# Kernel optimization log

Measured on AMD Instinct MI355X. Metric: run time of the kernel, lower is better.

The kernel has to match this reference:

```python
import jax, jax.numpy as jnp
import numpy as np
from jax import lax


def _conv(x, w, b, stride, pad):
    y = lax.conv_general_dilated(
        x, w, window_strides=(stride, stride),
        padding=[(pad, pad), (pad, pad)],
        dimension_numbers=('NCHW', 'OIHW', 'NCHW'))
    return y + b[None, :, None, None]


def _maxpool3s2(x):
    return lax.reduce_window(x, -jnp.inf, lax.max,
                             (1, 1, 3, 3), (1, 1, 2, 2), 'VALID')


def setup_inputs() -> dict:
    key = jax.random.key(0)
    ks = jax.random.split(key, 16)
    s = 0.05  # weight scale for numerical sanity
    inp = {
        'x': jax.random.normal(ks[0], (128, 3, 224, 224), jnp.float32),
        'w1': jax.random.normal(ks[1], (64, 3, 3, 3), jnp.float32) * s,
        'b1': jnp.zeros((64,), jnp.float32),
        'w2': jax.random.normal(ks[2], (192, 64, 5, 5), jnp.float32) * s,
        'b2': jnp.zeros((192,), jnp.float32),
        'w3': jax.random.normal(ks[3], (384, 192, 3, 3), jnp.float32) * s,
        'b3': jnp.zeros((384,), jnp.float32),
        'w4': jax.random.normal(ks[4], (256, 384, 3, 3), jnp.float32) * s,
        'b4': jnp.zeros((256,), jnp.float32),
        'w5': jax.random.normal(ks[5], (256, 256, 3, 3), jnp.float32) * s,
        'b5': jnp.zeros((256,), jnp.float32),
        'fc1_w': jax.random.normal(ks[6], (4096, 9216), jnp.float32) * 0.01,
        'fc1_b': jnp.zeros((4096,), jnp.float32),
        'fc2_w': jax.random.normal(ks[7], (4096, 4096), jnp.float32) * 0.01,
        'fc2_b': jnp.zeros((4096,), jnp.float32),
        'fc3_w': jax.random.normal(ks[8], (10, 4096), jnp.float32) * 0.01,
        'fc3_b': jnp.zeros((10,), jnp.float32),
        # uniform(0.1, 0.3) per element, matching random.uniform(0.1, 0.3)
        'unif': jax.random.uniform(ks[9], (128, 10), jnp.float32, 0.1, 0.3),
        # np.random.normal(0, 1) noise
        'noise': jax.random.normal(ks[10], (128, 10), jnp.float32),
    }
    return inp


def _forward(x, w1, b1, w2, b2, w3, b3, w4, b4, w5, b5,
             fc1_w, fc1_b, fc2_w, fc2_b, fc3_w, fc3_b, unif, noise):
    # features
    h = jax.nn.relu(_conv(x, w1, b1, stride=4, pad=2))   # [B,64,57,57]
    h = _maxpool3s2(h)                                   # [B,64,28,28]
    h = jax.nn.relu(_conv(h, w2, b2, stride=1, pad=2))   # [B,192,28,28]
    h = _maxpool3s2(h)                                   # [B,192,13,13]
    h = jax.nn.relu(_conv(h, w3, b3, stride=1, pad=1))   # [B,384,13,13]
    h = jax.nn.relu(_conv(h, w4, b4, stride=1, pad=1))   # [B,256,13,13]
    h = jax.nn.relu(_conv(h, w5, b5, stride=1, pad=1))   # [B,256,13,13]
    h = _maxpool3s2(h)                                   # [B,256,6,6]
    # adaptive avgpool to (6,6) is identity at this spatial size
    h = h.reshape(h.shape[0], 256 * 6 * 6)               # [B,9216]
    # classifier (Dropout = identity in eval mode)
    h = jax.nn.relu(h @ fc1_w.T + fc1_b)                 # [B,4096]
    h = jax.nn.relu(h @ fc2_w.T + fc2_b)                 # [B,4096]
    logits = h @ fc3_w.T + fc3_b                         # [B,10]
    # post: keep argmax entry, replace others with unif*max (detached),
    # add Gaussian noise, softmax
    m = jnp.max(logits, axis=-1, keepdims=True)          # [B,1]
    idx = jnp.argmax(logits, axis=-1, keepdims=True)     # first max, like torch
    onehot = jnp.arange(logits.shape[-1])[None, :] == idx
    filled = jnp.where(onehot, logits, unif * lax.stop_gradient(m))
    return jax.nn.softmax(filled + noise, axis=-1)


def reference(x, w1, b1, w2, b2, w3, b3, w4, b4, w5, b5,
              fc1_w, fc1_b, fc2_w, fc2_b, fc3_w, fc3_b, unif, noise):
    return _forward(x, w1, b1, w2, b2, w3, b3, w4, b4, w5, b5,
                    fc1_w, fc1_b, fc2_w, fc2_b, fc3_w, fc3_b, unif, noise)
```

## Files before the change

kernel.cpp:

```cpp
#include <hip/hip_runtime.h>
#include <math.h>


typedef __attribute__((ext_vector_type(4))) float  f32x4;
typedef __attribute__((ext_vector_type(8))) short  bf16x8;

#define OFF_C1O      25690112ull
#define OFF_X2H      0ull
#define OFF_X2L      12845056ull
#define OFF_WT2H     25690112ull
#define OFF_WT2L     26304512ull
#define OFF_WT3H     26918912ull
#define OFF_WT3L     28246016ull
#define OFF_WT4H     29573120ull
#define OFF_WT4L     31342592ull
#define OFF_WT5H     33112064ull
#define OFF_WT5L     34291712ull
#define OFF_Y2H      36000000ull
#define OFF_Y2L      74535168ull
#define OFF_X3H      113100000ull
#define OFF_X3L      121406688ull
#define OFF_Y3H      36000000ull
#define OFF_Y3L      52613376ull
#define OFF_Y4H      70000000ull
#define OFF_Y4L      81075584ull
#define OFF_Y5H      93000000ull
#define OFF_Y5L      104075584ull
#define OFF_P3       0ull
#define OFF_FC1      5000000ull
#define OFF_FC2      8000000ull
#define OFF_LOG      11000000ull
#define OFF_PART     40000000ull

__device__ inline void bf16split(float v, unsigned short& h, unsigned short& l) {
  unsigned u = __builtin_bit_cast(unsigned, v);
  unsigned hb = (u + 0x7fffu + ((u >> 16) & 1u)) >> 16;
  h = (unsigned short)hb;
  float hf = __builtin_bit_cast(float, hb << 16);
  float r = v - hf;
  unsigned u2 = __builtin_bit_cast(unsigned, r);
  l = (unsigned short)((u2 + 0x7fffu + ((u2 >> 16) & 1u)) >> 16);
}
__device__ inline void bf16split_fast(float v, unsigned short& h, unsigned short& l) {
  unsigned u = __builtin_bit_cast(unsigned, v);
  h = (unsigned short)(u >> 16);
  float r = v - __builtin_bit_cast(float, u & 0xFFFF0000u);
  unsigned u2 = __builtin_bit_cast(unsigned, r);
  l = (unsigned short)((u2 + 0x7fffu + ((u2 >> 16) & 1u)) >> 16);
}
__device__ inline float bf2f(unsigned short h) {
  return __builtin_bit_cast(float, ((unsigned)h) << 16);
}

__global__ __launch_bounds__(256) void conv1_kernel(
    const float* __restrict__ x, const float* __restrict__ w,
    const float* __restrict__ bias, float* __restrict__ out) {
  const int b = blockIdx.y;
  const int s = blockIdx.x * 256 + threadIdx.x;
  if (s >= 57 * 57) return;
  const int oh = s / 57, ow = s % 57;
  float iv[27];
#pragma unroll
  for (int ci = 0; ci < 3; ++ci)
#pragma unroll
    for (int kh = 0; kh < 3; ++kh)
#pragma unroll
      for (int kw = 0; kw < 3; ++kw) {
        const int ih = oh * 4 - 2 + kh;
        const int iw = ow * 4 - 2 + kw;
        float v = 0.f;
        if (ih >= 0 && ih < 224 && iw >= 0 && iw < 224)
          v = x[(((size_t)b * 3 + ci) * 224 + ih) * 224 + iw];
        iv[ci * 9 + kh * 3 + kw] = v;
      }
  for (int co = 0; co < 64; ++co) {
    float a = bias[co];
#pragma unroll
    for (int p = 0; p < 27; ++p) a = fmaf(w[co * 27 + p], iv[p], a);
    out[((size_t)b * 64 + co) * 3249 + s] = fmaxf(a, 0.f);
  }
}

__global__ __launch_bounds__(256) void pool1cvt_kernel(
    const float* __restrict__ in, unsigned short* __restrict__ xh,
    unsigned short* __restrict__ xl) {
  const int tid = blockIdx.x * 256 + threadIdx.x;
  if (tid >= 128 * 784) return;
  const int b = tid / 784, s = tid % 784;
  const int oh = s / 28, ow = s % 28;
  const float* base = in + (size_t)b * 64 * 3249 + (size_t)(oh * 2) * 57 + ow * 2;
  for (int cg = 0; cg < 16; ++cg) {
    unsigned short h[4], l[4];
#pragma unroll
    for (int j = 0; j < 4; ++j) {
      const float* p = base + (size_t)(cg * 4 + j) * 3249;
      float m = -INFINITY;
#pragma unroll
      for (int kh = 0; kh < 3; ++kh)
#pragma unroll
        for (int kw = 0; kw < 3; ++kw) m = fmaxf(m, p[kh * 57 + kw]);
      bf16split(m, h[j], l[j]);
    }
    const size_t g = ((size_t)b * 784 + s) * 64 + cg * 4;
    *reinterpret_cast<uint2*>(xh + g) =
        make_uint2((unsigned)h[0] | ((unsigned)h[1] << 16),
                   (unsigned)h[2] | ((unsigned)h[3] << 16));
    *reinterpret_cast<uint2*>(xl + g) =
        make_uint2((unsigned)l[0] | ((unsigned)l[1] << 16),
                   (unsigned)l[2] | ((unsigned)l[3] << 16));
  }
}

__global__ void wtrans_hl_kernel(const float* __restrict__ w,
                                 unsigned short* __restrict__ wh,
                                 unsigned short* __restrict__ wl,
                                 int C_in, int P, int C_out) {
  const int ncc = C_in >> 5;
  const int total = C_out * P * C_in;
  for (int e = blockIdx.x * blockDim.x + threadIdx.x; e < total;
       e += gridDim.x * blockDim.x) {
    const int ci_in = e & 31;
    int t1 = e >> 5;
    const int fr = t1 & 15;
    int t2 = t1 >> 4;
    const int cc = t2 % ncc;
    int t3 = t2 / ncc;
    const int p = t3 % P;
    const int ct = t3 / P;
    const int co = ct * 16 + fr;
    const int ci = cc * 32 + ci_in;
    const float v = w[((size_t)co * C_in + ci) * P + p];
    unsigned short h, l;
    bf16split(v, h, l);
    wh[e] = h; wl[e] = l;
  }
}

__global__ __launch_bounds__(256, 2) void conv2_mfma_kernel(
    const unsigned short* __restrict__ xh, const unsigned short* __restrict__ xl,
    const unsigned short* __restrict__ wh, const unsigned short* __restrict__ wl,
    const float* __restrict__ bias,
    unsigned short* __restrict__ yh, unsigned short* __restrict__ yl) {
  __shared__ unsigned short xt_h[352 * 40];
  __shared__ unsigned short xt_l[352 * 40];
  const int t = threadIdx.x;
  const int lane = t & 63, wv = t >> 6;
  const int b = blockIdx.x;
  const int rg = blockIdx.y;
  const int cg = blockIdx.z;
  const int fr = lane & 15, fq = lane >> 4;
  const int k0 = fq * 8;
  const int frag = fr * 32 + k0;

  int bofs[4];
  bool act[4];
#pragma unroll
  for (int ti = 0; ti < 4; ++ti) {
    const int tile = ti * 4 + wv;
    act[ti] = (tile <= 12);
    int n = tile * 16 + fr;
    if (tile > 12 || n > 195) n = 195;
    const int r = n / 28, c = n % 28;
    bofs[ti] = (r * 32 + c) * 40 + k0;
  }

  f32x4 acc[4][4];
#pragma unroll
  for (int i = 0; i < 4; ++i)
#pragma unroll
    for (int j = 0; j < 4; ++j) acc[i][j] = (f32x4){0.f, 0.f, 0.f, 0.f};

  for (int cc = 0; cc < 2; ++cc) {
    __syncthreads();
    for (int e = t; e < 1408; e += 256) {
      const int sp = e >> 2, kg = e & 3;
      const int hr = sp >> 5, hc = sp & 31;
      const int ih = rg * 7 + hr - 2, ic = hc - 2;
      uint4 vh = make_uint4(0, 0, 0, 0), vl = make_uint4(0, 0, 0, 0);
      if (ih >= 0 && ih < 28 && ic >= 0 && ic < 28) {
        const size_t g = ((size_t)b * 784 + ih * 28 + ic) * 64 + cc * 32 + kg * 8;
        vh = *reinterpret_cast<const uint4*>(xh + g);
        vl = *reinterpret_cast<const uint4*>(xl + g);
      }
      *reinterpret_cast<uint4*>(xt_h + sp * 40 + kg * 8) = vh;
      *reinterpret_cast<uint4*>(xt_l + sp * 40 + kg * 8) = vl;
    }
    __syncthreads();
#pragma unroll 5
    for (int p = 0; p < 25; ++p) {
      bf16x8 a_h[4], a_l[4];
#pragma unroll
      for (int cot = 0; cot < 4; ++cot) {
        const size_t wg = ((((size_t)(cg * 4 + cot) * 25 + p) * 2 + cc) << 9) + frag;
        a_h[cot] = __builtin_bit_cast(bf16x8, *reinterpret_cast<const uint4*>(wh + wg));
        a_l[cot] = __builtin_bit_cast(bf16x8, *reinterpret_cast<const uint4*>(wl + wg));
      }
      const int kh = p / 5, kw = p % 5;
      const int poff = (kh * 32 + kw) * 40;
      bf16x8 bh[4], bl[4];
#pragma unroll
      for (int ti = 0; ti < 4; ++ti) {
        if (act[ti]) {
          bh[ti] = __builtin_bit_cast(bf16x8,
              *reinterpret_cast<const uint4*>(xt_h + bofs[ti] + poff));
          bl[ti] = __builtin_bit_cast(bf16x8,
              *reinterpret_cast<const uint4*>(xt_l + bofs[ti] + poff));
        }
      }
#pragma unroll
      for (int ti = 0; ti < 4; ++ti) if (act[ti])
#pragma unroll
        for (int cot = 0; cot < 4; ++cot)
          acc[ti][cot] = __builtin_amdgcn_mfma_f32_16x16x32_bf16(a_h[cot], bh[ti], acc[ti][cot], 0, 0, 0);
#pragma unroll
      for (int ti = 0; ti < 4; ++ti) if (act[ti])
#pragma unroll
        for (int cot = 0; cot < 4; ++cot)
          acc[ti][cot] = __builtin_amdgcn_mfma_f32_16x16x32_bf16(a_h[cot], bl[ti], acc[ti][cot], 0, 0, 0);
#pragma unroll
      for (int ti = 0; ti < 4; ++ti) if (act[ti])
#pragma unroll
        for (int cot = 0; cot < 4; ++cot)
          acc[ti][cot] = __builtin_amdgcn_mfma_f32_16x16x32_bf16(a_l[cot], bh[ti], acc[ti][cot], 0, 0, 0);
    }
  }
#pragma unroll
  for (int cot = 0; cot < 4; ++cot) {
    const int co = cg * 64 + cot * 16 + fq * 4;
    const float4 bi = *reinterpret_cast<const float4*>(bias + co);
    const float bia[4] = {bi.x, bi.y, bi.z, bi.w};
#pragma unroll
    for (int ti = 0; ti < 4; ++ti) {
      const int tile = ti * 4 + wv;
      if (tile > 12) continue;
      const int n = tile * 16 + fr;
      if (n > 195) continue;
      const int oh = rg * 7 + n / 28, ow = n % 28;
      unsigned short h[4], l[4];
#pragma unroll
      for (int r = 0; r < 4; ++r) {
        const float v = fmaxf(acc[ti][cot][r] + bia[r], 0.f);
        bf16split(v, h[r], l[r]);
      }
      const size_t g = ((size_t)b * 784 + oh * 28 + ow) * 192 + co;
      *reinterpret_cast<uint2*>(yh + g) =
          make_uint2((unsigned)h[0] | ((unsigned)h[1] << 16),
                     (unsigned)h[2] | ((unsigned)h[3] << 16));
      *reinterpret_cast<uint2*>(yl + g) =
          make_uint2((unsigned)l[0] | ((unsigned)l[1] << 16),
                     (unsigned)l[2] | ((unsigned)l[3] << 16));
    }
  }
}

__global__ __launch_bounds__(256) void pool2_hl_kernel(
    const unsigned short* __restrict__ yh, const unsigned short* __restrict__ yl,
    unsigned short* __restrict__ xh, unsigned short* __restrict__ xl) {
  const int tid = blockIdx.x * 256 + threadIdx.x;
  if (tid >= 128 * 169 * 48) return;
  const int c4 = tid % 48;
  const int r = tid / 48;
  const int s = r % 169;
  const int b = r / 169;
  const int oh = s / 13, ow = s % 13;
  float m[4] = {-INFINITY, -INFINITY, -INFINITY, -INFINITY};
#pragma unroll
  for (int kh = 0; kh < 3; ++kh) {
#pragma unroll
    for (int kw = 0; kw < 3; ++kw) {
      const int si = (oh * 2 + kh) * 28 + (ow * 2 + kw);
      const size_t g = ((size_t)b * 784 + si) * 192 + c4 * 4;
      const uint2 vh = *reinterpret_cast<const uint2*>(yh + g);
      const uint2 vl = *reinterpret_cast<const uint2*>(yl + g);
      const unsigned hw[2] = {vh.x, vh.y}, lw[2] = {vl.x, vl.y};
#pragma unroll
      for (int j = 0; j < 4; ++j) {
        const float v = bf2f((unsigned short)(hw[j >> 1] >> ((j & 1) * 16))) +
                        bf2f((unsigned short)(lw[j >> 1] >> ((j & 1) * 16)));
        m[j] = fmaxf(m[j], v);
      }
    }
  }
  unsigned short h[4], l[4];
#pragma unroll
  for (int j = 0; j < 4; ++j) bf16split(m[j], h[j], l[j]);
  const size_t gd = ((size_t)b * 169 + s) * 192 + c4 * 4;
  *reinterpret_cast<uint2*>(xh + gd) =
      make_uint2((unsigned)h[0] | ((unsigned)h[1] << 16),
                 (unsigned)h[2] | ((unsigned)h[3] << 16));
  *reinterpret_cast<uint2*>(xl + gd) =
      make_uint2((unsigned)l[0] | ((unsigned)l[1] << 16),
                 (unsigned)l[2] | ((unsigned)l[3] << 16));
}

__global__ __launch_bounds__(256, 4) void conv13_mfma_kernel(
    const unsigned short* __restrict__ xh, const unsigned short* __restrict__ xl,
    const unsigned short* __restrict__ wh, const unsigned short* __restrict__ wl,
    const float* __restrict__ bias,
    unsigned short* __restrict__ yh, unsigned short* __restrict__ yl,
    int C_in, int C_out) {
  __shared__ unsigned short xt_h[225 * 40];
  __shared__ unsigned short xt_l[225 * 40];
  const int t = threadIdx.x;
  const int lane = t & 63;
  const int wv = t >> 6;
  const int b = blockIdx.x;
  const int co0 = blockIdx.y * 64 + wv * 16;
  const int ctile = blockIdx.y * 4 + wv;
  const int fr = lane & 15;
  const int fq = lane >> 4;
  const int k0 = fq * 8;
  const int frag = fr * 32 + k0;

  int bofs[11];
#pragma unroll
  for (int nt = 0; nt < 11; ++nt) {
    int n = nt * 16 + fr;
    if (n > 168) n = 168;
    const int oh = n / 13, ow = n % 13;
    bofs[nt] = (oh * 15 + ow) * 40 + k0;
  }

  f32x4 acc[11];
#pragma unroll
  for (int nt = 0; nt < 11; ++nt) acc[nt] = (f32x4){0.f, 0.f, 0.f, 0.f};

  const int ncc = C_in >> 5;
  for (int cc = 0; cc < ncc; ++cc) {
    __syncthreads();
    for (int e = t; e < 900; e += 256) {
      const int sp = e >> 2, kg = e & 3;
      const int r = sp / 15, c = sp % 15;
      const int ir = r - 1, ic = c - 1;
      uint4 vh = make_uint4(0, 0, 0, 0), vl = make_uint4(0, 0, 0, 0);
      if (ir >= 0 && ir < 13 && ic >= 0 && ic < 13) {
        const size_t g = ((size_t)b * 169 + ir * 13 + ic) * C_in + cc * 32 + kg * 8;
        vh = *reinterpret_cast<const uint4*>(xh + g);
        vl = *reinterpret_cast<const uint4*>(xl + g);
      }
      *reinterpret_cast<uint4*>(xt_h + sp * 40 + kg * 8) = vh;
      *reinterpret_cast<uint4*>(xt_l + sp * 40 + kg * 8) = vl;
    }
    __syncthreads();
#pragma unroll
    for (int p = 0; p < 9; ++p) {
      const size_t wg = ((((size_t)ctile * 9 + p) * ncc + cc) << 9) + frag;
      const bf16x8 ca_h = __builtin_bit_cast(bf16x8, *reinterpret_cast<const uint4*>(wh + wg));
      const bf16x8 ca_l = __builtin_bit_cast(bf16x8, *reinterpret_cast<const uint4*>(wl + wg));
      const int poff = ((p / 3) * 15 + (p % 3)) * 40;
#pragma unroll
      for (int q = 0; q < 3; ++q) {
        const int nq = (q < 2) ? 4 : 3;
        bf16x8 bh[4], bl[4];
#pragma unroll
        for (int i = 0; i < 4; ++i) {
          if (i < nq) {
            bh[i] = __builtin_bit_cast(bf16x8,
                *reinterpret_cast<const uint4*>(xt_h + bofs[q * 4 + i] + poff));
            bl[i] = __builtin_bit_cast(bf16x8,
                *reinterpret_cast<const uint4*>(xt_l + bofs[q * 4 + i] + poff));
          }
        }
#pragma unroll
        for (int i = 0; i < 4; ++i) if (i < nq)
          acc[q * 4 + i] = __builtin_amdgcn_mfma_f32_16x16x32_bf16(ca_h, bh[i], acc[q * 4 + i], 0, 0, 0);
#pragma unroll
        for (int i = 0; i < 4; ++i) if (i < nq)
          acc[q * 4 + i] = __builtin_amdgcn_mfma_f32_16x16x32_bf16(ca_h, bl[i], acc[q * 4 + i], 0, 0, 0);
#pragma unroll
        for (int i = 0; i < 4; ++i) if (i < nq)
          acc[q * 4 + i] = __builtin_amdgcn_mfma_f32_16x16x32_bf16(ca_l, bh[i], acc[q * 4 + i], 0, 0, 0);
      }
    }
  }
  const int co_w = co0 + fq * 4;
  const float4 bi = *reinterpret_cast<const float4*>(bias + co_w);
  const float bia[4] = {bi.x, bi.y, bi.z, bi.w};
#pragma unroll
  for (int nt = 0; nt < 11; ++nt) {
    const int n = nt * 16 + fr;
    if (n > 168) continue;
    unsigned short h[4], l[4];
#pragma unroll
    for (int r = 0; r < 4; ++r) {
      float v = fmaxf(acc[nt][r] + bia[r], 0.f);
      bf16split(v, h[r], l[r]);
    }
    const size_t g = ((size_t)b * 169 + n) * C_out + co_w;
    *reinterpret_cast<uint2*>(yh + g) =
        make_uint2((unsigned)h[0] | ((unsigned)h[1] << 16),
                   (unsigned)h[2] | ((unsigned)h[3] << 16));
    *reinterpret_cast<uint2*>(yl + g) =
        make_uint2((unsigned)l[0] | ((unsigned)l[1] << 16),
                   (unsigned)l[2] | ((unsigned)l[3] << 16));
  }
}

__global__ __launch_bounds__(256) void pool3_hl_kernel(
    const unsigned short* __restrict__ yh, const unsigned short* __restrict__ yl,
    float* __restrict__ out) {
  const int b = blockIdx.x;
  const int s2 = blockIdx.y;
  const int c = threadIdx.x;
  const int oh = s2 / 6, ow = s2 % 6;
  float m = -INFINITY;
#pragma unroll
  for (int kh = 0; kh < 3; ++kh)
#pragma unroll
    for (int kw = 0; kw < 3; ++kw) {
      const int si = (oh * 2 + kh) * 13 + (ow * 2 + kw);
      const size_t g = ((size_t)b * 169 + si) * 256 + c;
      m = fmaxf(m, bf2f(yh[g]) + bf2f(yl[g]));
    }
  out[((size_t)b * 256 + c) * 36 + s2] = m;
}

__global__ __launch_bounds__(256, 2) void fc_mfma_kernel(
    const float* __restrict__ act, const float* __restrict__ Wm,
    float* __restrict__ part, int K, int kchunk, int Cout) {
  __shared__ unsigned short ah[128 * 40];
  __shared__ unsigned short al[128 * 40];
  const int t = threadIdx.x;
  const int lane = t & 63, wv = t >> 6;
  const int m0 = blockIdx.x * 128 + wv * 32;
  const int kb = blockIdx.y * kchunk;
  const int fr = lane & 15, fq = lane >> 4;

  f32x4 acc[2][8];
#pragma unroll
  for (int i = 0; i < 2; ++i)
#pragma unroll
    for (int j = 0; j < 8; ++j) acc[i][j] = (f32x4){0.f, 0.f, 0.f, 0.f};

  for (int kc = kb; kc < kb + kchunk; kc += 32) {
    __syncthreads();
#pragma unroll
    for (int i = 0; i < 4; ++i) {
      const int u = t + i * 256;
      const int n = u >> 3, j = u & 7;
      const float4 v = *reinterpret_cast<const float4*>(act + (size_t)n * K + kc + j * 4);
      const float vv[4] = {v.x, v.y, v.z, v.w};
      unsigned short h[4], l[4];
#pragma unroll
      for (int q = 0; q < 4; ++q) bf16split_fast(vv[q], h[q], l[q]);
      *reinterpret_cast<uint2*>(ah + n * 40 + j * 4) =
          make_uint2((unsigned)h[0] | ((unsigned)h[1] << 16),
                     (unsigned)h[2] | ((unsigned)h[3] << 16));
      *reinterpret_cast<uint2*>(al + n * 40 + j * 4) =
          make_uint2((unsigned)l[0] | ((unsigned)l[1] << 16),
                     (unsigned)l[2] | ((unsigned)l[3] << 16));
    }
    __syncthreads();
    bf16x8 a_h[2], a_l[2];
#pragma unroll
    for (int mt = 0; mt < 2; ++mt) {
      const float* wp = Wm + (size_t)(m0 + mt * 16 + fr) * K + kc + fq * 8;
      const float4 w0 = *reinterpret_cast<const float4*>(wp);
      const float4 w1 = *reinterpret_cast<const float4*>(wp + 4);
      const float ws[8] = {w0.x, w0.y, w0.z, w0.w, w1.x, w1.y, w1.z, w1.w};
#pragma unroll
      for (int q = 0; q < 8; ++q) {
        unsigned short h, l;
        bf16split_fast(ws[q], h, l);
        a_h[mt][q] = (short)h;
        a_l[mt][q] = (short)l;
      }
    }
#pragma unroll
    for (int np = 0; np < 4; ++np) {
      bf16x8 bh[2], bl[2];
#pragma unroll
      for (int i = 0; i < 2; ++i) {
        const int nt = np * 2 + i;
        bh[i] = __builtin_bit_cast(bf16x8,
            *reinterpret_cast<const uint4*>(ah + (nt * 16 + fr) * 40 + fq * 8));
        bl[i] = __builtin_bit_cast(bf16x8,
            *reinterpret_cast<const uint4*>(al + (nt * 16 + fr) * 40 + fq * 8));
      }
#pragma unroll
      for (int i = 0; i < 2; ++i)
#pragma unroll
        for (int mt = 0; mt < 2; ++mt)
          acc[mt][np * 2 + i] = __builtin_amdgcn_mfma_f32_16x16x32_bf16(a_h[mt], bh[i], acc[mt][np * 2 + i], 0, 0, 0);
#pragma unroll
      for (int i = 0; i < 2; ++i)
#pragma unroll
        for (int mt = 0; mt < 2; ++mt)
          acc[mt][np * 2 + i] = __builtin_amdgcn_mfma_f32_16x16x32_bf16(a_h[mt], bl[i], acc[mt][np * 2 + i], 0, 0, 0);
#pragma unroll
      for (int i = 0; i < 2; ++i)
#pragma unroll
        for (int mt = 0; mt < 2; ++mt)
          acc[mt][np * 2 + i] = __builtin_amdgcn_mfma_f32_16x16x32_bf16(a_l[mt], bh[i], acc[mt][np * 2 + i], 0, 0, 0);
    }
  }
  const size_t base = (size_t)blockIdx.y * Cout * 128;
#pragma unroll
  for (int mt = 0; mt < 2; ++mt) {
#pragma unroll
    for (int nt = 0; nt < 8; ++nt) {
#pragma unroll
      for (int r = 0; r < 4; ++r) {
        const int m = m0 + mt * 16 + fq * 4 + r;
        const int n = nt * 16 + fr;
        part[base + (size_t)m * 128 + n] = acc[mt][nt][r];
      }
    }
  }
}

__global__ __launch_bounds__(256) void fc_reduce_kernel(
    const float* __restrict__ part, const float* __restrict__ bias,
    float* __restrict__ out, int Cout, int KS, int relu) {
  const int g = blockIdx.x * 256 + threadIdx.x;
  if (g >= Cout * 128) return;
  const int n = g & 127, m = g >> 7;
  float s = 0.f;
  for (int ks = 0; ks < KS; ++ks)
    s += part[(size_t)ks * Cout * 128 + (size_t)m * 128 + n];
  s += bias[m];
  if (relu) s = fmaxf(s, 0.f);
  out[(size_t)n * Cout + m] = s;
}

__global__ __launch_bounds__(256) void fc3_kernel(
    const float* __restrict__ A, const float* __restrict__ W,
    const float* __restrict__ bias, float* __restrict__ out) {
  __shared__ float red[256];
  const int b = blockIdx.x;
  const int t = threadIdx.x;
  float acc[10];
#pragma unroll
  for (int n = 0; n < 10; ++n) acc[n] = 0.f;
  const float* a = A + (size_t)b * 4096;
  for (int k = t; k < 4096; k += 256) {
    const float av = a[k];
#pragma unroll
    for (int n = 0; n < 10; ++n) acc[n] = fmaf(av, W[n * 4096 + k], acc[n]);
  }
  for (int n = 0; n < 10; ++n) {
    red[t] = acc[n];
    __syncthreads();
    for (int off = 128; off > 0; off >>= 1) {
      if (t < off) red[t] += red[t + off];
      __syncthreads();
    }
    if (t == 0) out[b * 10 + n] = red[0] + bias[n];
    __syncthreads();
  }
}

__global__ void post_kernel(const float* __restrict__ logits,
                            const float* __restrict__ unif,
                            const float* __restrict__ noise,
                            float* __restrict__ out) {
  const int b = blockIdx.x * blockDim.x + threadIdx.x;
  if (b >= 128) return;
  float lg[10];
#pragma unroll
  for (int j = 0; j < 10; ++j) lg[j] = logits[b * 10 + j];
  float m = lg[0];
  int idx = 0;
#pragma unroll
  for (int j = 1; j < 10; ++j) {
    if (lg[j] > m) { m = lg[j]; idx = j; }
  }
  float v[10];
#pragma unroll
  for (int j = 0; j < 10; ++j)
    v[j] = ((j == idx) ? lg[j] : unif[b * 10 + j] * m) + noise[b * 10 + j];
  float mx = v[0];
#pragma unroll
  for (int j = 1; j < 10; ++j) mx = fmaxf(mx, v[j]);
  float sum = 0.f;
#pragma unroll
  for (int j = 0; j < 10; ++j) { v[j] = expf(v[j] - mx); sum += v[j]; }
  const float inv = 1.f / sum;
#pragma unroll
  for (int j = 0; j < 10; ++j) out[b * 10 + j] = v[j] * inv;
}

extern "C" void kernel_launch(void* const* d_in, const int* in_sizes, int n_in,
                              void* d_out, int out_size, void* d_ws, size_t ws_size,
                              hipStream_t stream) {
  const float* x     = (const float*)d_in[0];
  const float* w1    = (const float*)d_in[1];
  const float* b1    = (const float*)d_in[2];
  const float* w2    = (const float*)d_in[3];
  const float* b2    = (const float*)d_in[4];
  const float* w3    = (const float*)d_in[5];
  const float* b3    = (const float*)d_in[6];
  const float* w4    = (const float*)d_in[7];
  const float* b4    = (const float*)d_in[8];
  const float* w5    = (const float*)d_in[9];
  const float* b5    = (const float*)d_in[10];
  const float* fc1_w = (const float*)d_in[11];
  const float* fc1_b = (const float*)d_in[12];
  const float* fc2_w = (const float*)d_in[13];
  const float* fc2_b = (const float*)d_in[14];
  const float* fc3_w = (const float*)d_in[15];
  const float* fc3_b = (const float*)d_in[16];
  const float* unif  = (const float*)d_in[17];
  const float* noise = (const float*)d_in[18];
  float* out = (float*)d_out;

  char* W = (char*)d_ws;
#define FP(off) ((float*)(W + (off)))
#define US(off) ((unsigned short*)(W + (off)))

  conv1_kernel<<<dim3(13, 128), 256, 0, stream>>>(x, w1, b1, FP(OFF_C1O));
  pool1cvt_kernel<<<392, 256, 0, stream>>>(FP(OFF_C1O), US(OFF_X2H), US(OFF_X2L));
  wtrans_hl_kernel<<<512, 256, 0, stream>>>(w2, US(OFF_WT2H), US(OFF_WT2L), 64, 25, 192);
  wtrans_hl_kernel<<<512, 256, 0, stream>>>(w3, US(OFF_WT3H), US(OFF_WT3L), 192, 9, 384);
  wtrans_hl_kernel<<<512, 256, 0, stream>>>(w4, US(OFF_WT4H), US(OFF_WT4L), 384, 9, 256);
  wtrans_hl_kernel<<<512, 256, 0, stream>>>(w5, US(OFF_WT5H), US(OFF_WT5L), 256, 9, 256);
  conv2_mfma_kernel<<<dim3(128, 4, 3), 256, 0, stream>>>(
      US(OFF_X2H), US(OFF_X2L), US(OFF_WT2H), US(OFF_WT2L), b2,
      US(OFF_Y2H), US(OFF_Y2L));
  pool2_hl_kernel<<<4056, 256, 0, stream>>>(
      US(OFF_Y2H), US(OFF_Y2L), US(OFF_X3H), US(OFF_X3L));
  conv13_mfma_kernel<<<dim3(128, 6), 256, 0, stream>>>(
      US(OFF_X3H), US(OFF_X3L), US(OFF_WT3H), US(OFF_WT3L), b3,
      US(OFF_Y3H), US(OFF_Y3L), 192, 384);
  conv13_mfma_kernel<<<dim3(128, 4), 256, 0, stream>>>(
      US(OFF_Y3H), US(OFF_Y3L), US(OFF_WT4H), US(OFF_WT4L), b4,
      US(OFF_Y4H), US(OFF_Y4L), 384, 256);
  conv13_mfma_kernel<<<dim3(128, 4), 256, 0, stream>>>(
      US(OFF_Y4H), US(OFF_Y4L), US(OFF_WT5H), US(OFF_WT5L), b5,
      US(OFF_Y5H), US(OFF_Y5L), 256, 256);
  pool3_hl_kernel<<<dim3(128, 36), 256, 0, stream>>>(US(OFF_Y5H), US(OFF_Y5L), FP(OFF_P3));
  fc_mfma_kernel<<<dim3(32, 16), 256, 0, stream>>>(FP(OFF_P3), fc1_w, FP(OFF_PART), 9216, 576, 4096);
  fc_reduce_kernel<<<2048, 256, 0, stream>>>(FP(OFF_PART), fc1_b, FP(OFF_FC1), 4096, 16, 1);
  fc_mfma_kernel<<<dim3(32, 16), 256, 0, stream>>>(FP(OFF_FC1), fc2_w, FP(OFF_PART), 4096, 256, 4096);
  fc_reduce_kernel<<<2048, 256, 0, stream>>>(FP(OFF_PART), fc2_b, FP(OFF_FC2), 4096, 16, 1);
  fc3_kernel<<<128, 256, 0, stream>>>(FP(OFF_FC2), fc3_w, fc3_b, FP(OFF_LOG));
  post_kernel<<<1, 128, 0, stream>>>(FP(OFF_LOG), unif, noise, out);
}
```

Measured before the change: 740.4 us.

## Fuse conv1 with maxpool1 and bf16 split, recomputing overlapping conv outputs

Replaces the separate conv1 and pool1/convert kernels with one kernel that computes conv1 outputs for each 3x3 pooling window in registers, takes the max, applies ReLU and writes the hi/lo bf16 split directly. This removes the large fp32 conv1 intermediate write and reread. Each thread handles half of the 64 channels for one pooled pixel, which recomputes overlapping conv outputs at roughly twice the arithmetic and repeats the input reads.

```diff
diff --git a/kernel.cpp b/kernel.cpp
--- a/kernel.cpp
+++ b/kernel.cpp
@@ -5,7 +5,6 @@
 typedef __attribute__((ext_vector_type(4))) float  f32x4;
 typedef __attribute__((ext_vector_type(8))) short  bf16x8;
 
-#define OFF_C1O      25690112ull
 #define OFF_X2H      0ull
 #define OFF_X2L      12845056ull
 #define OFF_WT2H     25690112ull
@@ -52,56 +51,54 @@
   return __builtin_bit_cast(float, ((unsigned)h) << 16);
 }
 
-__global__ __launch_bounds__(256) void conv1_kernel(
+__global__ __launch_bounds__(256, 2) void conv1pool_kernel(
     const float* __restrict__ x, const float* __restrict__ w,
-    const float* __restrict__ bias, float* __restrict__ out) {
-  const int b = blockIdx.y;
-  const int s = blockIdx.x * 256 + threadIdx.x;
-  if (s >= 57 * 57) return;
-  const int oh = s / 57, ow = s % 57;
-  float iv[27];
-#pragma unroll
-  for (int ci = 0; ci < 3; ++ci)
-#pragma unroll
-    for (int kh = 0; kh < 3; ++kh)
-#pragma unroll
-      for (int kw = 0; kw < 3; ++kw) {
-        const int ih = oh * 4 - 2 + kh;
-        const int iw = ow * 4 - 2 + kw;
-        float v = 0.f;
-        if (ih >= 0 && ih < 224 && iw >= 0 && iw < 224)
-          v = x[(((size_t)b * 3 + ci) * 224 + ih) * 224 + iw];
-        iv[ci * 9 + kh * 3 + kw] = v;
-      }
-  for (int co = 0; co < 64; ++co) {
-    float a = bias[co];
-#pragma unroll
-    for (int p = 0; p < 27; ++p) a = fmaf(w[co * 27 + p], iv[p], a);
-    out[((size_t)b * 64 + co) * 3249 + s] = fmaxf(a, 0.f);
-  }
-}
-
-__global__ __launch_bounds__(256) void pool1cvt_kernel(
-    const float* __restrict__ in, unsigned short* __restrict__ xh,
-    unsigned short* __restrict__ xl) {
+    const float* __restrict__ bias,
+    unsigned short* __restrict__ xh, unsigned short* __restrict__ xl) {
   const int tid = blockIdx.x * 256 + threadIdx.x;
-  if (tid >= 128 * 784) return;
-  const int b = tid / 784, s = tid % 784;
+  if (tid >= 128 * 784 * 2) return;
+  const int half = tid & 1;
+  const int r = tid >> 1;
+  const int s = r % 784;
+  const int b = r / 784;
   const int oh = s / 28, ow = s % 28;
-  const float* base = in + (size_t)b * 64 * 3249 + (size_t)(oh * 2) * 57 + ow * 2;
-  for (int cg = 0; cg < 16; ++cg) {
+  const int co0 = half * 32;
+
+  float m[32];
+#pragma unroll
+  for (int j = 0; j < 32; ++j) m[j] = -INFINITY;
+
+  for (int q = 0; q < 9; ++q) {
+    const int qh = oh * 2 + q / 3;
+    const int qw = ow * 2 + q % 3;
+    float iv[27];
+#pragma unroll
+    for (int ci = 0; ci < 3; ++ci)
+#pragma unroll
+      for (int kh = 0; kh < 3; ++kh)
+#pragma unroll
+        for (int kw = 0; kw < 3; ++kw) {
+          const int ih = qh * 4 - 2 + kh;
+          const int iw = qw * 4 - 2 + kw;
+          float v = 0.f;
+          if (ih >= 0 && ih < 224 && iw >= 0 && iw < 224)
+            v = x[(((size_t)b * 3 + ci) * 224 + ih) * 224 + iw];
+          iv[ci * 9 + kh * 3 + kw] = v;
+        }
+    for (int j = 0; j < 32; ++j) {
+      float a = bias[co0 + j];
+#pragma unroll
+      for (int p = 0; p < 27; ++p) a = fmaf(w[(co0 + j) * 27 + p], iv[p], a);
+      m[j] = fmaxf(m[j], a);
+    }
+  }
+#pragma unroll
+  for (int cg = 0; cg < 8; ++cg) {
     unsigned short h[4], l[4];
 #pragma unroll
-    for (int j = 0; j < 4; ++j) {
-      const float* p = base + (size_t)(cg * 4 + j) * 3249;
-      float m = -INFINITY;
-#pragma unroll
-      for (int kh = 0; kh < 3; ++kh)
-#pragma unroll
-        for (int kw = 0; kw < 3; ++kw) m = fmaxf(m, p[kh * 57 + kw]);
-      bf16split(m, h[j], l[j]);
-    }
-    const size_t g = ((size_t)b * 784 + s) * 64 + cg * 4;
+    for (int j = 0; j < 4; ++j)
+      bf16split(fmaxf(m[cg * 4 + j], 0.f), h[j], l[j]);
+    const size_t g = ((size_t)b * 784 + s) * 64 + co0 + cg * 4;
     *reinterpret_cast<uint2*>(xh + g) =
         make_uint2((unsigned)h[0] | ((unsigned)h[1] << 16),
                    (unsigned)h[2] | ((unsigned)h[3] << 16));
@@ -608,8 +605,7 @@
 #define FP(off) ((float*)(W + (off)))
 #define US(off) ((unsigned short*)(W + (off)))
 
-  conv1_kernel<<<dim3(13, 128), 256, 0, stream>>>(x, w1, b1, FP(OFF_C1O));
-  pool1cvt_kernel<<<392, 256, 0, stream>>>(FP(OFF_C1O), US(OFF_X2H), US(OFF_X2L));
+  conv1pool_kernel<<<784, 256, 0, stream>>>(x, w1, b1, US(OFF_X2H), US(OFF_X2L));
   wtrans_hl_kernel<<<512, 256, 0, stream>>>(w2, US(OFF_WT2H), US(OFF_WT2L), 64, 25, 192);
   wtrans_hl_kernel<<<512, 256, 0, stream>>>(w3, US(OFF_WT3H), US(OFF_WT3L), 192, 9, 384);
   wtrans_hl_kernel<<<512, 256, 0, stream>>>(w4, US(OFF_WT4H), US(OFF_WT4L), 384, 9, 256);
```

Result: slower. 1.160 ms (+56.7%).
